# Performance work log

Hardware: AMD Instinct MI355X
Metric: run time of the kernel (lower is better)

## Reference

```python
import jax, jax.numpy as jnp
import numpy as np

B, T, D_IN, D_OUT, H = 2, 2048, 1024, 1024, 16
HD = D_OUT // H


def setup_inputs() -> dict:
    key = jax.random.key(0)
    ks = jax.random.split(key, 6)
    s_in = 1.0 / np.sqrt(D_IN)
    s_out = 1.0 / np.sqrt(D_OUT)
    return {
        "x": jax.random.normal(ks[0], (B, T, D_IN), dtype=jnp.float32),
        # torch nn.Linear stores weight as (out_features, in_features)
        "Wq": jax.random.uniform(ks[1], (D_OUT, D_IN), jnp.float32, -s_in, s_in),
        "Wk": jax.random.uniform(ks[2], (D_OUT, D_IN), jnp.float32, -s_in, s_in),
        "Wv": jax.random.uniform(ks[3], (D_OUT, D_IN), jnp.float32, -s_in, s_in),
        "Wo": jax.random.uniform(ks[4], (D_OUT, D_OUT), jnp.float32, -s_out, s_out),
        "bo": jax.random.uniform(ks[5], (D_OUT,), jnp.float32, -s_out, s_out),
    }


def reference(x, Wq, Wk, Wv, Wo, bo):
    b, t, _ = x.shape
    q = jnp.einsum("btd,ed->bte", x, Wq).reshape(b, t, H, HD).transpose(0, 2, 1, 3)
    k = jnp.einsum("btd,ed->bte", x, Wk).reshape(b, t, H, HD).transpose(0, 2, 1, 3)
    v = jnp.einsum("btd,ed->bte", x, Wv).reshape(b, t, H, HD).transpose(0, 2, 1, 3)
    # [b, h, q, k] materialized scores, masked then scaled (as in source)
    scores = jnp.einsum("bhqd,bhkd->bhqk", q, k)
    causal = jnp.triu(jnp.ones((t, t), dtype=bool), k=1)
    scores = jnp.where(causal, -jnp.inf, scores)
    attn = jax.nn.softmax(scores / jnp.sqrt(jnp.float32(HD)), axis=-1)
    ctx = jnp.einsum("bhqk,bhkd->bhqd", attn, v)
    # NOTE: the source does .view(b, t, d_out) WITHOUT transposing (b,h,t,hd)
    # back to (b,t,h,hd). We replicate that reshape faithfully.
    ctx = ctx.reshape(b, t, D_OUT)
    return jnp.einsum("btd,ed->bte", ctx, Wo) + bo
```

## Files before the change

### kernel.cpp

```cpp
#include <hip/hip_runtime.h>
#include <math.h>

#define BB 2
#define TT 2048
#define DD 1024
#define NH 16
#define HDD 64

typedef __attribute__((ext_vector_type(8))) short v8s;
typedef __attribute__((ext_vector_type(4))) short v4s;
typedef __attribute__((ext_vector_type(4))) float f32x4;

__device__ __forceinline__ unsigned short f2bf(float f) {
    union { float f; unsigned int u; } c; c.f = f;
    unsigned int r = c.u + 0x7FFF + ((c.u >> 16) & 1);
    return (unsigned short)(r >> 16);
}

__device__ __forceinline__ v4s pack_bf16x4(float a, float b, float c, float d) {
#if __has_builtin(__builtin_amdgcn_cvt_pk_bf16_f32)
    auto lo = __builtin_amdgcn_cvt_pk_bf16_f32(a, b);
    auto hi = __builtin_amdgcn_cvt_pk_bf16_f32(c, d);
    union { v4s v; struct { decltype(lo) l; decltype(hi) h; } p; } u;
    u.p.l = lo; u.p.h = hi;
    return u.v;
#else
    v4s r;
    r[0] = (short)f2bf(a); r[1] = (short)f2bf(b);
    r[2] = (short)f2bf(c); r[3] = (short)f2bf(d);
    return r;
#endif
}

__device__ __forceinline__ float fexp2(float x) {
#if __has_builtin(__builtin_amdgcn_exp2f)
    return __builtin_amdgcn_exp2f(x);
#else
    float r; asm("v_exp_f32 %0, %1" : "=v"(r) : "v"(x)); return r;
#endif
}

__device__ __forceinline__ void gload_lds16(const void* g, void* l) {
    __builtin_amdgcn_global_load_lds(
        (const __attribute__((address_space(1))) void*)g,
        (__attribute__((address_space(3))) void*)l, 16, 0, 0);
}

__device__ __forceinline__ f32x4 mfma16x16x16bf16(v4s a, v4s b, f32x4 c) {
#if __has_builtin(__builtin_amdgcn_mfma_f32_16x16x16bf16_1k)
    return __builtin_amdgcn_mfma_f32_16x16x16bf16_1k(a, b, c, 0, 0, 0);
#else
    f32x4 d;
    asm("v_mfma_f32_16x16x16_bf16 %0, %1, %2, %0"
        : "=v"(d) : "v"(a), "v"(b), "0"(c));
    return d;
#endif
}

__global__ __launch_bounds__(256) void cast5_kernel(
    const float* __restrict__ x, const float* __restrict__ wq,
    const float* __restrict__ wk, const float* __restrict__ wv,
    const float* __restrict__ wo,
    unsigned short* __restrict__ xo, unsigned short* __restrict__ wqo,
    unsigned short* __restrict__ wko, unsigned short* __restrict__ wvo,
    unsigned short* __restrict__ woo)
{
    const float* s; unsigned short* d; int n4;
    switch (blockIdx.y) {
        case 0: s = x;  d = xo;  n4 = BB * TT * DD / 4; break;
        case 1: s = wq; d = wqo; n4 = DD * DD / 4; break;
        case 2: s = wk; d = wko; n4 = DD * DD / 4; break;
        case 3: s = wv; d = wvo; n4 = DD * DD / 4; break;
        default: s = wo; d = woo; n4 = DD * DD / 4; break;
    }
    int i = blockIdx.x * 256 + threadIdx.x;
    if (i < n4) {
        float4 v = ((const float4*)s)[i];
        ushort4 o;
        o.x = f2bf(v.x); o.y = f2bf(v.y); o.z = f2bf(v.z); o.w = f2bf(v.w);
        ((ushort4*)d)[i] = o;
    }
}

__global__ __launch_bounds__(256, 5) void qkv_mfma(
    const unsigned short* __restrict__ x,
    const unsigned short* __restrict__ wq, const unsigned short* __restrict__ wk,
    const unsigned short* __restrict__ wv,
    unsigned short* __restrict__ qo, unsigned short* __restrict__ ko,
    unsigned short* __restrict__ vo)
{
    __shared__ unsigned short SMEM[12288];

    const int tid = threadIdx.x;
    const int lane = tid & 63;
    const int wid = tid >> 6;
    const int l15 = lane & 15, quad = lane >> 4;

    const int m0 = blockIdx.x << 7;
    const int ny = blockIdx.y;
    const int which = ny >> 4;
    const int n0 = (ny & 15) << 6;
    const unsigned short* W = (which == 0) ? wq : (which == 1) ? wk : wv;

    const int wm = (wid >> 1) << 6;
    const int wn = (wid & 1) << 5;

    const int srow = tid >> 2;
    const int cs = (tid & 3) << 3;
    const int csw = cs ^ (((srow >> 1) & 3) << 3);
    const int fA = tid << 4;
    const int rcol = ((quad ^ ((l15 >> 1) & 3)) << 4);

    char* const smem = (char*)SMEM;

#define QKV_STAGE(k0, buf)                                                     \
    do {                                                                       \
        gload_lds16(&x[(size_t)(m0 + srow) * DD + (k0) + csw],                 \
                    smem + (buf) * 8192 + fA);                                 \
        gload_lds16(&x[(size_t)(m0 + srow + 64) * DD + (k0) + csw],            \
                    smem + (buf) * 8192 + fA + 4096);                          \
        gload_lds16(&W[(size_t)(n0 + srow) * DD + (k0) + csw],                 \
                    smem + 16384 + (buf) * 4096 + fA);                         \
    } while (0)

    f32x4 acc[4][2] = {};

    QKV_STAGE(0, 0);
    __syncthreads();

    int cur = 0;
    for (int k0 = 0; k0 < DD; k0 += 32) {
        if (k0 + 32 < DD) QKV_STAGE(k0 + 32, cur ^ 1);

        const char* Ab = smem + cur * 8192;
        const char* Bb = smem + 16384 + cur * 4096;
        v8s af[4], bf[2];
#pragma unroll
        for (int i = 0; i < 4; ++i)
            af[i] = *(const v8s*)(Ab + (wm + (i << 4) + l15) * 64 + rcol);
#pragma unroll
        for (int j = 0; j < 2; ++j)
            bf[j] = *(const v8s*)(Bb + (wn + (j << 4) + l15) * 64 + rcol);
#pragma unroll
        for (int i = 0; i < 4; ++i)
#pragma unroll
            for (int j = 0; j < 2; ++j)
                acc[i][j] = __builtin_amdgcn_mfma_f32_16x16x32_bf16(af[i], bf[j], acc[i][j], 0, 0, 0);

        __syncthreads();
        cur ^= 1;
    }
#undef QKV_STAGE

    if (which == 2) {
#pragma unroll
        for (int i = 0; i < 4; ++i)
#pragma unroll
            for (int j = 0; j < 2; ++j) {
                const int n = n0 + wn + (j << 4) + l15;
                const int h = n >> 6, hd = n & 63;
                const int mb = m0 + wm + (i << 4) + (quad << 2);
                const int b = mb >> 11, t = mb & 2047;
                ushort4 pk;
                pk.x = f2bf(acc[i][j][0]); pk.y = f2bf(acc[i][j][1]);
                pk.z = f2bf(acc[i][j][2]); pk.w = f2bf(acc[i][j][3]);
                *(ushort4*)&vo[((((size_t)(b * NH + h) << 6) + hd) << 11) + t] = pk;
            }
    } else {
        unsigned short* outp = (which == 0) ? qo : ko;
        const float sc = (which == 1) ? 0.18033688011112042f : 1.0f;
#pragma unroll
        for (int p = 0; p < 2; ++p) {
            __syncthreads();
            if ((wid >> 1) == p) {
#pragma unroll
                for (int i = 0; i < 4; ++i)
#pragma unroll
                    for (int j = 0; j < 2; ++j)
#pragma unroll
                        for (int r = 0; r < 4; ++r) {
                            const int row = (i << 4) + (quad << 2) + r;
                            SMEM[row * 72 + wn + (j << 4) + l15] = f2bf(acc[i][j][r] * sc);
                        }
            }
            __syncthreads();
            const int rr = tid >> 2;
            const int cg = (tid & 3) << 4;
            const int m = m0 + (p << 6) + rr;
            const int b = m >> 11, t = m & 2047;
#pragma unroll
            for (int k2 = 0; k2 < 2; ++k2) {
                const int col = cg + (k2 << 3);
                const int n = n0 + col;
                const int h = n >> 6, hd = n & 63;
                const uint4 val = *(const uint4*)&SMEM[rr * 72 + col];
                *(uint4*)&outp[(((size_t)(b * NH + h) * TT + t) << 6) + hd] = val;
            }
        }
    }
}

__global__ __launch_bounds__(256) void attn_mfma(
    const unsigned short* __restrict__ q, const unsigned short* __restrict__ k,
    const unsigned short* __restrict__ vt, unsigned short* __restrict__ ctx)
{
    __shared__ unsigned short Qs[64][64];
    __shared__ unsigned short Ks[2][64][64];
    __shared__ unsigned short Vts[2][64][64];

    const int tid = threadIdx.x;
    const int lane = tid & 63;
    const int wid = tid >> 6;
    const int l15 = lane & 15, quad = lane >> 4;
    const int r7 = (l15 & 7) << 3;

    const int bh = blockIdx.x;
    const int qt = 31 - (int)blockIdx.y;
    const int q0 = qt << 6;
    const int qrow = q0 + (wid << 4) + l15;

    const unsigned short* qb = q + (size_t)bh * TT * HDD;
    const unsigned short* kb = k + (size_t)bh * TT * HDD;
    const unsigned short* vb = vt + (size_t)bh * HDD * TT;
    unsigned short* cb = ctx + (size_t)bh * TT * HDD;

    const int cr = tid >> 3;
    const int cc = (tid & 7) << 3;
    const int cs = cc ^ ((cr & 7) << 3);

#pragma unroll
    for (int u = 0; u < 2; ++u) {
        const int r = cr + (u << 5);
        *(uint4*)&Qs[r][cs] = *(const uint4*)&qb[(size_t)(q0 + r) * HDD + cc];
    }
    {
        uint4 k0r = *(const uint4*)&kb[(size_t)cr * HDD + cc];
        uint4 k1r = *(const uint4*)&kb[(size_t)(cr + 32) * HDD + cc];
        uint4 v0r = *(const uint4*)&vb[((size_t)cr << 11) + cc];
        uint4 v1r = *(const uint4*)&vb[((size_t)(cr + 32) << 11) + cc];
        *(uint4*)&Ks[0][cr][cs] = k0r;
        *(uint4*)&Ks[0][cr + 32][cs] = k1r;
        *(uint4*)&Vts[0][cr][cs] = v0r;
        *(uint4*)&Vts[0][cr + 32][cs] = v1r;
    }
    __syncthreads();

    v8s qf[2];
#pragma unroll
    for (int c = 0; c < 2; ++c)
        qf[c] = *(const v8s*)&Qs[(wid << 4) + l15]
                               [(((c << 5) + (quad << 3)) ^ r7)];

    float m_i = -INFINITY, l_i = 0.f;
    f32x4 o[4] = {};

    for (int jt = 0; jt <= qt; ++jt) {
        const int cur = jt & 1;

        uint4 k0r, k1r, v0r, v1r;
        const bool pre = (jt < qt);
        if (pre) {
            const int kn = (jt + 1) << 6;
            k0r = *(const uint4*)&kb[(size_t)(kn + cr) * HDD + cc];
            k1r = *(const uint4*)&kb[(size_t)(kn + cr + 32) * HDD + cc];
            v0r = *(const uint4*)&vb[((size_t)cr << 11) + kn + cc];
            v1r = *(const uint4*)&vb[((size_t)(cr + 32) << 11) + kn + cc];
        }

        const int k0 = jt << 6;

        f32x4 s[4] = {};
        const int kc0 = (quad << 3) ^ r7;
#pragma unroll
        for (int m = 0; m < 4; ++m) {
            const v8s kf0 = *(const v8s*)&Ks[cur][(m << 4) + l15][kc0];
            const v8s kf1 = *(const v8s*)&Ks[cur][(m << 4) + l15][kc0 ^ 32];
            s[m] = __builtin_amdgcn_mfma_f32_16x16x32_bf16(kf0, qf[0], s[m], 0, 0, 0);
            s[m] = __builtin_amdgcn_mfma_f32_16x16x32_bf16(kf1, qf[1], s[m], 0, 0, 0);
        }

        if (jt == qt) {
#pragma unroll
            for (int m = 0; m < 4; ++m) {
                const int kc = k0 + (m << 4) + (quad << 2);
#pragma unroll
                for (int r = 0; r < 4; ++r)
                    if (kc + r > qrow) s[m][r] = -INFINITY;
            }
        }

        float mx = fmaxf(fmaxf(s[0][0], s[0][1]), fmaxf(s[0][2], s[0][3]));
        mx = fmaxf(mx, fmaxf(fmaxf(s[1][0], s[1][1]), fmaxf(s[1][2], s[1][3])));
        mx = fmaxf(mx, fmaxf(fmaxf(s[2][0], s[2][1]), fmaxf(s[2][2], s[2][3])));
        mx = fmaxf(mx, fmaxf(fmaxf(s[3][0], s[3][1]), fmaxf(s[3][2], s[3][3])));
        mx = fmaxf(mx, __shfl_xor(mx, 16));
        mx = fmaxf(mx, __shfl_xor(mx, 32));
        const float m_new = fmaxf(m_i, mx);
        const float alpha = fexp2(m_i - m_new);
        m_i = m_new;

        float sum = 0.f;
        v4s pf[4];
#pragma unroll
        for (int m = 0; m < 4; ++m) {
            const float p0 = fexp2(s[m][0] - m_new);
            const float p1 = fexp2(s[m][1] - m_new);
            const float p2 = fexp2(s[m][2] - m_new);
            const float p3 = fexp2(s[m][3] - m_new);
            sum += (p0 + p1) + (p2 + p3);
            pf[m] = pack_bf16x4(p0, p1, p2, p3);
        }
        sum += __shfl_xor(sum, 16);
        sum += __shfl_xor(sum, 32);
        l_i = l_i * alpha + sum;

#pragma unroll
        for (int m = 0; m < 4; ++m)
#pragma unroll
            for (int r = 0; r < 4; ++r)
                o[m][r] *= alpha;

#pragma unroll
        for (int m = 0; m < 4; ++m)
#pragma unroll
            for (int c = 0; c < 4; ++c) {
                const v4s vf = *(const v4s*)&Vts[cur][(m << 4) + l15]
                                                    [(((c << 4) + (quad << 2)) ^ r7)];
                o[m] = mfma16x16x16bf16(vf, pf[c], o[m]);
            }

        if (pre) {
            const int nxt = cur ^ 1;
            *(uint4*)&Ks[nxt][cr][cs] = k0r;
            *(uint4*)&Ks[nxt][cr + 32][cs] = k1r;
            *(uint4*)&Vts[nxt][cr][cs] = v0r;
            *(uint4*)&Vts[nxt][cr + 32][cs] = v1r;
        }
        __syncthreads();
    }

    const float linv = 1.f / l_i;
#pragma unroll
    for (int m = 0; m < 4; ++m) {
        ushort4 st;
        st.x = f2bf(o[m][0] * linv); st.y = f2bf(o[m][1] * linv);
        st.z = f2bf(o[m][2] * linv); st.w = f2bf(o[m][3] * linv);
        *(ushort4*)&cb[((size_t)qrow << 6) + (m << 4) + (quad << 2)] = st;
    }
}

__global__ __launch_bounds__(256) void oproj_mfma(
    const unsigned short* __restrict__ c, const unsigned short* __restrict__ wo,
    const float* __restrict__ bo, float* __restrict__ out)
{
    __shared__ unsigned short SMEM[12288];

    const int tid = threadIdx.x;
    const int lane = tid & 63;
    const int wid = tid >> 6;
    const int l15 = lane & 15, quad = lane >> 4;

    const int m0 = blockIdx.x << 7;
    const int n0 = blockIdx.y << 6;
    const int wm = (wid >> 1) << 6;
    const int wn = (wid & 1) << 5;

    const int srow = tid >> 2;
    const int cs = (tid & 3) << 3;
    const int csw = cs ^ (((srow >> 1) & 3) << 3);
    const int fA = tid << 4;
    const int rcol = ((quad ^ ((l15 >> 1) & 3)) << 4);

    char* const smem = (char*)SMEM;

#define OP_STAGE(k0, buf)                                                      \
    do {                                                                       \
        gload_lds16(&c[(size_t)(m0 + srow) * DD + (k0) + csw],                 \
                    smem + (buf) * 8192 + fA);                                 \
        gload_lds16(&c[(size_t)(m0 + srow + 64) * DD + (k0) + csw],            \
                    smem + (buf) * 8192 + fA + 4096);                          \
        gload_lds16(&wo[(size_t)(n0 + srow) * DD + (k0) + csw],                \
                    smem + 16384 + (buf) * 4096 + fA);                         \
    } while (0)

    f32x4 acc[4][2] = {};

    OP_STAGE(0, 0);
    __syncthreads();

    int cur = 0;
    for (int k0 = 0; k0 < DD; k0 += 32) {
        if (k0 + 32 < DD) OP_STAGE(k0 + 32, cur ^ 1);

        const char* Ab = smem + cur * 8192;
        const char* Bb = smem + 16384 + cur * 4096;
        v8s af[4], bf[2];
#pragma unroll
        for (int i = 0; i < 4; ++i)
            af[i] = *(const v8s*)(Ab + (wm + (i << 4) + l15) * 64 + rcol);
#pragma unroll
        for (int j = 0; j < 2; ++j)
            bf[j] = *(const v8s*)(Bb + (wn + (j << 4) + l15) * 64 + rcol);
#pragma unroll
        for (int i = 0; i < 4; ++i)
#pragma unroll
            for (int j = 0; j < 2; ++j)
                acc[i][j] = __builtin_amdgcn_mfma_f32_16x16x32_bf16(af[i], bf[j], acc[i][j], 0, 0, 0);

        __syncthreads();
        cur ^= 1;
    }
#undef OP_STAGE

#pragma unroll
    for (int j = 0; j < 2; ++j) {
        const int n = n0 + wn + (j << 4) + l15;
        const float bias = bo[n];
#pragma unroll
        for (int i = 0; i < 4; ++i) {
            const int mb = m0 + wm + (i << 4) + (quad << 2);
#pragma unroll
            for (int r = 0; r < 4; ++r)
                out[(size_t)(mb + r) * DD + n] = acc[i][j][r] + bias;
        }
    }
}

extern "C" void kernel_launch(void* const* d_in, const int* in_sizes, int n_in,
                              void* d_out, int out_size, void* d_ws, size_t ws_size,
                              hipStream_t stream) {
    const float* x  = (const float*)d_in[0];
    const float* Wq = (const float*)d_in[1];
    const float* Wk = (const float*)d_in[2];
    const float* Wv = (const float*)d_in[3];
    const float* Wo = (const float*)d_in[4];
    const float* bo = (const float*)d_in[5];
    float* out = (float*)d_out;

    const size_t NX = (size_t)BB * TT * DD;
    const size_t NW = (size_t)DD * DD;

    unsigned short* xb  = (unsigned short*)d_ws;
    unsigned short* wqb = xb + NX;
    unsigned short* wkb = wqb + NW;
    unsigned short* wvb = wkb + NW;
    unsigned short* wob = wvb + NW;
    unsigned short* qb  = wob + NW;
    unsigned short* kb  = qb + NX;
    unsigned short* vtb = kb + NX;
    unsigned short* cbuf = vtb + NX;

    cast5_kernel<<<dim3(4096, 5), 256, 0, stream>>>(x, Wq, Wk, Wv, Wo,
                                                    xb, wqb, wkb, wvb, wob);
    qkv_mfma<<<dim3(32, 48), 256, 0, stream>>>(xb, wqb, wkb, wvb, qb, kb, vtb);
    attn_mfma<<<dim3(32, 32), 256, 0, stream>>>(qb, kb, vtb, cbuf);
    oproj_mfma<<<dim3(32, 16), 256, 0, stream>>>(cbuf, wob, bo, out);
}
```

Baseline: 184.7 us.

## Double GEMM K-tile to 64 with XOR-swizzled LDS and trim cast grid

After: 169.3 us. 8.3% less time.

```diff
diff --git a/kernel.cpp b/kernel.cpp
--- a/kernel.cpp
+++ b/kernel.cpp
@@ -65,36 +65,48 @@
     unsigned short* __restrict__ wko, unsigned short* __restrict__ wvo,
     unsigned short* __restrict__ woo)
 {
-    const float* s; unsigned short* d; int n4;
-    switch (blockIdx.y) {
-        case 0: s = x;  d = xo;  n4 = BB * TT * DD / 4; break;
-        case 1: s = wq; d = wqo; n4 = DD * DD / 4; break;
-        case 2: s = wk; d = wko; n4 = DD * DD / 4; break;
-        case 3: s = wv; d = wvo; n4 = DD * DD / 4; break;
-        default: s = wo; d = woo; n4 = DD * DD / 4; break;
-    }
-    int i = blockIdx.x * 256 + threadIdx.x;
-    if (i < n4) {
-        float4 v = ((const float4*)s)[i];
+    const int tid = blockIdx.x * 256 + threadIdx.x;
+    if (blockIdx.y == 0) {
+        const int n4 = BB * TT * DD / 4;
+#pragma unroll
+        for (int p = 0; p < 4; ++p) {
+            const int i = tid + (p << 18);
+            if (i < n4) {
+                float4 v = ((const float4*)x)[i];
+                ushort4 o;
+                o.x = f2bf(v.x); o.y = f2bf(v.y); o.z = f2bf(v.z); o.w = f2bf(v.w);
+                ((ushort4*)xo)[i] = o;
+            }
+        }
+    } else {
+        const float* s; unsigned short* d;
+        switch (blockIdx.y) {
+            case 1: s = wq; d = wqo; break;
+            case 2: s = wk; d = wko; break;
+            case 3: s = wv; d = wvo; break;
+            default: s = wo; d = woo; break;
+        }
+        float4 v = ((const float4*)s)[tid];
         ushort4 o;
         o.x = f2bf(v.x); o.y = f2bf(v.y); o.z = f2bf(v.z); o.w = f2bf(v.w);
-        ((ushort4*)d)[i] = o;
-    }
-}
-
-__global__ __launch_bounds__(256, 5) void qkv_mfma(
+        ((ushort4*)d)[tid] = o;
+    }
+}
+
+__global__ __launch_bounds__(256, 3) void qkv_mfma(
     const unsigned short* __restrict__ x,
     const unsigned short* __restrict__ wq, const unsigned short* __restrict__ wk,
     const unsigned short* __restrict__ wv,
     unsigned short* __restrict__ qo, unsigned short* __restrict__ ko,
     unsigned short* __restrict__ vo)
 {
-    __shared__ unsigned short SMEM[12288];
+    __shared__ unsigned short SMEM[24576];
 
     const int tid = threadIdx.x;
     const int lane = tid & 63;
     const int wid = tid >> 6;
     const int l15 = lane & 15, quad = lane >> 4;
+    const int l7 = l15 & 7;
 
     const int m0 = blockIdx.x << 7;
     const int ny = blockIdx.y;
@@ -105,22 +117,24 @@
     const int wm = (wid >> 1) << 6;
     const int wn = (wid & 1) << 5;
 
-    const int srow = tid >> 2;
-    const int cs = (tid & 3) << 3;
-    const int csw = cs ^ (((srow >> 1) & 3) << 3);
-    const int fA = tid << 4;
-    const int rcol = ((quad ^ ((l15 >> 1) & 3)) << 4);
-
     char* const smem = (char*)SMEM;
 
 #define QKV_STAGE(k0, buf)                                                     \
     do {                                                                       \
-        gload_lds16(&x[(size_t)(m0 + srow) * DD + (k0) + csw],                 \
-                    smem + (buf) * 8192 + fA);                                 \
-        gload_lds16(&x[(size_t)(m0 + srow + 64) * DD + (k0) + csw],            \
-                    smem + (buf) * 8192 + fA + 4096);                          \
-        gload_lds16(&W[(size_t)(n0 + srow) * DD + (k0) + csw],                 \
-                    smem + 16384 + (buf) * 4096 + fA);                         \
+        _Pragma("unroll") for (int p = 0; p < 4; ++p) {                        \
+            const int f = (tid << 4) + (p << 12);                              \
+            const int r = f >> 7;                                              \
+            const int gc = ((((f >> 4) & 7) ^ (r & 7)) << 3);                  \
+            gload_lds16(&x[(size_t)(m0 + r) * DD + (k0) + gc],                 \
+                        smem + (buf) * 16384 + f);                             \
+        }                                                                      \
+        _Pragma("unroll") for (int p = 0; p < 2; ++p) {                        \
+            const int f = (tid << 4) + (p << 12);                              \
+            const int r = f >> 7;                                              \
+            const int gc = ((((f >> 4) & 7) ^ (r & 7)) << 3);                  \
+            gload_lds16(&W[(size_t)(n0 + r) * DD + (k0) + gc],                 \
+                        smem + 32768 + (buf) * 8192 + f);                      \
+        }                                                                      \
     } while (0)
 
     f32x4 acc[4][2] = {};
@@ -129,23 +143,28 @@
     __syncthreads();
 
     int cur = 0;
-    for (int k0 = 0; k0 < DD; k0 += 32) {
-        if (k0 + 32 < DD) QKV_STAGE(k0 + 32, cur ^ 1);
-
-        const char* Ab = smem + cur * 8192;
-        const char* Bb = smem + 16384 + cur * 4096;
-        v8s af[4], bf[2];
-#pragma unroll
-        for (int i = 0; i < 4; ++i)
-            af[i] = *(const v8s*)(Ab + (wm + (i << 4) + l15) * 64 + rcol);
-#pragma unroll
-        for (int j = 0; j < 2; ++j)
-            bf[j] = *(const v8s*)(Bb + (wn + (j << 4) + l15) * 64 + rcol);
-#pragma unroll
-        for (int i = 0; i < 4; ++i)
+    for (int k0 = 0; k0 < DD; k0 += 64) {
+        if (k0 + 64 < DD) QKV_STAGE(k0 + 64, cur ^ 1);
+
+        const char* Ab = smem + cur * 16384;
+        const char* Bb = smem + 32768 + cur * 8192;
+#pragma unroll
+        for (int h = 0; h < 2; ++h) {
+            const int rc = (((h << 2) + quad) ^ l7) << 4;
+            v8s af[4], bf[2];
+#pragma unroll
+            for (int i = 0; i < 4; ++i)
+                af[i] = *(const v8s*)(Ab + (wm + (i << 4) + l15) * 128 + rc);
 #pragma unroll
             for (int j = 0; j < 2; ++j)
-                acc[i][j] = __builtin_amdgcn_mfma_f32_16x16x32_bf16(af[i], bf[j], acc[i][j], 0, 0, 0);
+                bf[j] = *(const v8s*)(Bb + (wn + (j << 4) + l15) * 128 + rc);
+#pragma unroll
+            for (int i = 0; i < 4; ++i)
+#pragma unroll
+                for (int j = 0; j < 2; ++j)
+                    acc[i][j] = __builtin_amdgcn_mfma_f32_16x16x32_bf16(
+                        af[i], bf[j], acc[i][j], 0, 0, 0);
+        }
 
         __syncthreads();
         cur ^= 1;
@@ -349,38 +368,41 @@
     }
 }
 
-__global__ __launch_bounds__(256) void oproj_mfma(
+__global__ __launch_bounds__(256, 3) void oproj_mfma(
     const unsigned short* __restrict__ c, const unsigned short* __restrict__ wo,
     const float* __restrict__ bo, float* __restrict__ out)
 {
-    __shared__ unsigned short SMEM[12288];
+    __shared__ unsigned short SMEM[24576];
 
     const int tid = threadIdx.x;
     const int lane = tid & 63;
     const int wid = tid >> 6;
     const int l15 = lane & 15, quad = lane >> 4;
+    const int l7 = l15 & 7;
 
     const int m0 = blockIdx.x << 7;
     const int n0 = blockIdx.y << 6;
     const int wm = (wid >> 1) << 6;
     const int wn = (wid & 1) << 5;
 
-    const int srow = tid >> 2;
-    const int cs = (tid & 3) << 3;
-    const int csw = cs ^ (((srow >> 1) & 3) << 3);
-    const int fA = tid << 4;
-    const int rcol = ((quad ^ ((l15 >> 1) & 3)) << 4);
-
     char* const smem = (char*)SMEM;
 
 #define OP_STAGE(k0, buf)                                                      \
     do {                                                                       \
-        gload_lds16(&c[(size_t)(m0 + srow) * DD + (k0) + csw],                 \
-                    smem + (buf) * 8192 + fA);                                 \
-        gload_lds16(&c[(size_t)(m0 + srow + 64) * DD + (k0) + csw],            \
-                    smem + (buf) * 8192 + fA + 4096);                          \
-        gload_lds16(&wo[(size_t)(n0 + srow) * DD + (k0) + csw],                \
-                    smem + 16384 + (buf) * 4096 + fA);                         \
+        _Pragma("unroll") for (int p = 0; p < 4; ++p) {                        \
+            const int f = (tid << 4) + (p << 12);                              \
+            const int r = f >> 7;                                              \
+            const int gc = ((((f >> 4) & 7) ^ (r & 7)) << 3);                  \
+            gload_lds16(&c[(size_t)(m0 + r) * DD + (k0) + gc],                 \
+                        smem + (buf) * 16384 + f);                             \
+        }                                                                      \
+        _Pragma("unroll") for (int p = 0; p < 2; ++p) {                        \
+            const int f = (tid << 4) + (p << 12);                              \
+            const int r = f >> 7;                                              \
+            const int gc = ((((f >> 4) & 7) ^ (r & 7)) << 3);                  \
+            gload_lds16(&wo[(size_t)(n0 + r) * DD + (k0) + gc],                \
+                        smem + 32768 + (buf) * 8192 + f);                      \
+        }                                                                      \
     } while (0)
 
     f32x4 acc[4][2] = {};
@@ -389,23 +411,28 @@
     __syncthreads();
 
     int cur = 0;
-    for (int k0 = 0; k0 < DD; k0 += 32) {
-        if (k0 + 32 < DD) OP_STAGE(k0 + 32, cur ^ 1);
-
-        const char* Ab = smem + cur * 8192;
-        const char* Bb = smem + 16384 + cur * 4096;
-        v8s af[4], bf[2];
-#pragma unroll
-        for (int i = 0; i < 4; ++i)
-            af[i] = *(const v8s*)(Ab + (wm + (i << 4) + l15) * 64 + rcol);
-#pragma unroll
-        for (int j = 0; j < 2; ++j)
-            bf[j] = *(const v8s*)(Bb + (wn + (j << 4) + l15) * 64 + rcol);
-#pragma unroll
-        for (int i = 0; i < 4; ++i)
+    for (int k0 = 0; k0 < DD; k0 += 64) {
+        if (k0 + 64 < DD) OP_STAGE(k0 + 64, cur ^ 1);
+
+        const char* Ab = smem + cur * 16384;
+        const char* Bb = smem + 32768 + cur * 8192;
+#pragma unroll
+        for (int h = 0; h < 2; ++h) {
+            const int rc = (((h << 2) + quad) ^ l7) << 4;
+            v8s af[4], bf[2];
+#pragma unroll
+            for (int i = 0; i < 4; ++i)
+                af[i] = *(const v8s*)(Ab + (wm + (i << 4) + l15) * 128 + rc);
 #pragma unroll
             for (int j = 0; j < 2; ++j)
-                acc[i][j] = __builtin_amdgcn_mfma_f32_16x16x32_bf16(af[i], bf[j], acc[i][j], 0, 0, 0);
+                bf[j] = *(const v8s*)(Bb + (wn + (j << 4) + l15) * 128 + rc);
+#pragma unroll
+            for (int i = 0; i < 4; ++i)
+#pragma unroll
+                for (int j = 0; j < 2; ++j)
+                    acc[i][j] = __builtin_amdgcn_mfma_f32_16x16x32_bf16(
+                        af[i], bf[j], acc[i][j], 0, 0, 0);
+        }
 
         __syncthreads();
         cur ^= 1;
@@ -450,7 +477,7 @@
     unsigned short* vtb = kb + NX;
     unsigned short* cbuf = vtb + NX;
 
-    cast5_kernel<<<dim3(4096, 5), 256, 0, stream>>>(x, Wq, Wk, Wv, Wo,
+    cast5_kernel<<<dim3(1024, 5), 256, 0, stream>>>(x, Wq, Wk, Wv, Wo,
                                                     xb, wqb, wkb, wvb, wob);
     qkv_mfma<<<dim3(32, 48), 256, 0, stream>>>(xb, wqb, wkb, wvb, qb, kb, vtb);
     attn_mfma<<<dim3(32, 32), 256, 0, stream>>>(qb, kb, vtb, cbuf);
```
